# Optimization experiments

Measured on AMD Instinct MI355X. Metric: run time of the kernel, lower is better.

The kernel has to match this reference:

```python
import jax, jax.numpy as jnp
import numpy as np

N_S, N_G, D, K = 30000, 3000, 128, 16
SIGMA = 2.5
BOX = 60.0  # Angstrom box for random coordinates


def setup_inputs() -> dict:
    key = jax.random.key(0)
    ks = jax.random.split(key, 10)
    s = 1.0 / np.sqrt(D)
    return {
        'xs': jax.random.normal(ks[0], (N_S, D), jnp.float32),
        'xg': jax.random.normal(ks[1], (N_G, D), jnp.float32),
        'pos_s': jax.random.uniform(ks[2], (N_S, 3), jnp.float32) * BOX,
        'pos_g': jax.random.uniform(ks[3], (N_G, 3), jnp.float32) * BOX,
        'W_s_pre': jax.random.normal(ks[4], (D, D), jnp.float32) * s,
        'W_g_pre': jax.random.normal(ks[5], (D, D), jnp.float32) * s,
        'W_gs': jax.random.normal(ks[6], (D, D), jnp.float32) * s,
        'W_sg': jax.random.normal(ks[7], (D, D), jnp.float32) * s,
        'W_s_post': jax.random.normal(ks[8], (2 * D, D), jnp.float32) * s,
        'W_g_post': jax.random.normal(ks[9], (2 * D, D), jnp.float32) * s,
        'k': K,
    }


def reference(xs, xg, pos_s, pos_g, W_s_pre, W_g_pre, W_gs, W_sg, W_s_post, W_g_post, k):
    n_s, d = xs.shape
    # ---- compute_bipartite_graphs: knn of each graph node over surface nodes ----
    # squared pairwise distances via gemm form: (N_G, N_S)
    d2 = ((pos_g ** 2).sum(-1)[:, None] + (pos_s ** 2).sum(-1)[None, :]
          - 2.0 * pos_g @ pos_s.T)
    neg_d2, idx = jax.lax.top_k(-d2, k)          # idx: (N_G, K) surface neighbors
    w = jnp.exp(neg_d2 / (2.0 * SIGMA ** 2))     # RBF edge weight exp(-d^2/(2*sigma^2))
    # ---- pre blocks ----
    hs = xs @ W_s_pre                             # (N_S, D)
    hg = xg @ W_g_pre                             # (N_G, D)
    # ---- bp_gs block: graph -> surface weighted edge-conv (scatter-add) ----
    msg_gs = (hg @ W_gs)[:, None, :] * w[:, :, None]          # (N_G, K, D)
    xs_out = jnp.zeros((n_s, d), hs.dtype).at[idx.reshape(-1)].add(
        msg_gs.reshape(-1, d))
    # ---- bp_sg block: surface -> graph weighted edge-conv (gather-sum) ----
    xg_out = ((hs @ W_sg)[idx] * w[:, :, None]).sum(axis=1)   # (N_G, D)
    # ---- post blocks: combine pre features with message output ----
    xs_new = jax.nn.relu(jnp.concatenate([hs, xs_out], axis=-1) @ W_s_post)
    xg_new = jax.nn.relu(jnp.concatenate([hg, xg_out], axis=-1) @ W_g_post)
    return xs_new, xg_new
```

## Files before the change

kernel.cpp:

```cpp
#include <hip/hip_runtime.h>
#include <stdint.h>

#define N_S 30000
#define N_G 3000
#define DD  128
#define KK  16
#define NE  (N_G * KK)
#define NC  16
#define CELLS (NC * NC * NC)
#define CH  3.75f
#define CAP 16
#define SURV 192
#define ECAP 32
#define EOVF_CAP 8192

#define FILL_BLOCKS 118
#define PACK_BLOCKS 384
#define NBS16 1875
#define NBG16 188
#define PRE_TILES (NBS16 + NBG16)
#define GROUPS 1032
#define GRID3 (GROUPS * 5)
#define NBS 469
#define NBG 47
#define NTILE (NBS + NBG)

typedef unsigned long long ull;
#define INF_KEY 0x7F7FFFFF7FFFFFFFull

using v8s = __attribute__((ext_vector_type(8))) short;
using v4f = __attribute__((ext_vector_type(4))) float;

__device__ __forceinline__ float bf2f(unsigned short u) {
    union { unsigned int i; float f; } v; v.i = ((unsigned int)u) << 16; return v.f;
}
__device__ __forceinline__ unsigned short f2bf(float f) {
    union { float f; unsigned int i; } v; v.f = f;
    unsigned int x = v.i;
    return (unsigned short)((x + 0x7fffu + ((x >> 16) & 1u)) >> 16);
}
__device__ __forceinline__ float ldIn(const void* p, int i, int bf) {
    return bf ? bf2f(((const unsigned short*)p)[i]) : ((const float*)p)[i];
}
__device__ __forceinline__ void stOut(void* p, int i, float v, int bf) {
    if (bf) ((unsigned short*)p)[i] = f2bf(v);
    else    ((float*)p)[i] = v;
}
__device__ __forceinline__ int cellOf(float x) {
    int c = (int)(x * (1.0f / CH));
    if (c < 0) c = 0; if (c > NC - 1) c = NC - 1;
    return c;
}
__device__ __forceinline__ float dist2(float gx, float gy, float gz, float4 cd) {
    const float dx = gx - cd.x, dy = gy - cd.y, dz = gz - cd.z;
    return fmaf(dx, dx, fmaf(dy, dy, dz * dz));
}
__device__ __forceinline__ ull packKey(float d2, int sid) {
    return ((ull)__float_as_uint(d2) << 32) | (unsigned)sid;
}

__device__ __forceinline__ int detectFlag(const void* pos_g) {
    const unsigned int* w = (const unsigned int*)pos_g;
    int votes = 0;
#pragma unroll
    for (int i = 0; i < 16; ++i) {
        const unsigned int b = (w[i] >> 8) & 0xFFu;
        votes += (b >= 0x3Eu && b <= 0x42u) ? 1 : 0;
    }
    return votes >= 8;
}

__device__ __forceinline__ void emitEdge(int g, ull key, int rank,
                                         int* __restrict__ idx_out,
                                         float* __restrict__ w_out,
                                         int* __restrict__ scnt,
                                         int2* __restrict__ edge,
                                         int4* __restrict__ eovf,
                                         int* __restrict__ neovf)
{
    const int sid = (int)(unsigned)key;
    const float d2 = __uint_as_float((unsigned)(key >> 32));
    const float wv = expf(-d2 * (1.0f / 12.5f));
    idx_out[g * KK + rank] = sid;
    w_out[g * KK + rank] = wv;
    const int c = atomicAdd(&scnt[sid], 1);
    if (c < ECAP) {
        edge[(size_t)sid * ECAP + c] = make_int2(g, __float_as_int(wv));
    } else {
        const int o = atomicAdd(neovf, 1);
        if (o < EOVF_CAP) eovf[o] = make_int4(sid, g, __float_as_int(wv), 0);
    }
}

__device__ __forceinline__ void ins16(ull key, ull bk[KK]) {
    if (key >= bk[KK - 1]) return;
    ull c = key;
#pragma unroll
    for (int j = 0; j < KK; ++j) {
        const bool less = c < bk[j];
        const ull nk = less ? c : bk[j];
        const ull ok = less ? bk[j] : c;
        bk[j] = nk; c = ok;
    }
}

__device__ bool knn_fast(int g, int bf, const void* pos_g,
                         const int* __restrict__ ccnt,
                         const float4* __restrict__ scell,
                         const float4* __restrict__ ovf, int novf,
                         int* __restrict__ idx_out, float* __restrict__ w_out,
                         int* __restrict__ scnt, int2* __restrict__ edge,
                         int4* __restrict__ eovf, int* __restrict__ neovf,
                         ull* __restrict__ skey)
{
    const int t = threadIdx.x;

    const float gx = ldIn(pos_g, 3 * g + 0, bf);
    const float gy = ldIn(pos_g, 3 * g + 1, bf);
    const float gz = ldIn(pos_g, 3 * g + 2, bf);
    const int cx = cellOf(gx), cy = cellOf(gy), cz = cellOf(gz);

    float m = 1e30f;
    if (cx - 1 > 0)      m = fminf(m, gx - (float)(cx - 1) * CH);
    if (cx + 1 < NC - 1) m = fminf(m, (float)(cx + 2) * CH - gx);
    if (cy - 1 > 0)      m = fminf(m, gy - (float)(cy - 1) * CH);
    if (cy + 1 < NC - 1) m = fminf(m, (float)(cy + 2) * CH - gy);
    if (cz - 1 > 0)      m = fminf(m, gz - (float)(cz - 1) * CH);
    if (cz + 1 < NC - 1) m = fminf(m, (float)(cz + 2) * CH - gz);
    m = fmaxf(m, 0.f);
    const float m2eff = (m < 1e29f) ? m * m * (1.0f - 1e-5f) : 1e30f;

    int cnt = 0, base = 0;
    if (t < 54) {
        const int cell = t >> 1, h = t & 1;
        const int dx = cell / 9 - 1, dy = (cell / 3) % 3 - 1, dz = cell % 3 - 1;
        const int X = cx + dx, Y = cy + dy, Z = cz + dz;
        if (X >= 0 && X < NC && Y >= 0 && Y < NC && Z >= 0 && Z < NC) {
            const int cid = (X * NC + Y) * NC + Z;
            int c = ccnt[cid]; if (c > CAP) c = CAP;
            const int lo = h * 8;
            const int hi = (c < lo + 8) ? c : (lo + 8);
            cnt = (hi > lo) ? (hi - lo) : 0;
            base = cid * CAP + lo;
        }
    }

    ull kv[8]; int okm = 0;
#pragma unroll
    for (int i = 0; i < 8; ++i) {
        kv[i] = 0;
        if (i < cnt) {
            const float4 cd = scell[base + i];
            const float d2 = dist2(gx, gy, gz, cd);
            if (d2 < m2eff) { okm |= (1 << i); kv[i] = packKey(d2, __float_as_int(cd.w)); }
        }
    }
    int myc = __popc(okm);
    int incl = myc;
    for (int d = 1; d < 64; d <<= 1) {
        int v = __shfl_up(incl, d);
        if (t >= d) incl += v;
    }
    int total = __shfl(incl, 63);
    int pos = incl - myc;
#pragma unroll
    for (int i = 0; i < 8; ++i) {
        if (okm & (1 << i)) {
            if (pos < SURV) skey[pos] = kv[i];
            ++pos;
        }
    }

    for (int i0 = 0; i0 < novf; i0 += 64) {
        const int i = i0 + t;
        bool act = (i < novf);
        ull key = 0;
        if (act) {
            const float4 cd = ovf[i];
            const float d2 = dist2(gx, gy, gz, cd);
            act = (d2 < m2eff);
            if (act) key = packKey(d2, __float_as_int(cd.w));
        }
        const ull b = __ballot(act);
        const int p2 = total + (int)__popcll(b & ((1ull << t) - 1ull));
        if (act && p2 < SURV) skey[p2] = key;
        total += (int)__popcll(b);
    }

    if (total < KK || total > SURV) return false;
    __syncthreads();

    const int n = total;
    ull ki[3]; int rk[3]; int nv = 0;
    for (int i = t; i < n && nv < 3; i += 64) { ki[nv] = skey[i]; rk[nv] = 0; ++nv; }
    for (int j = 0; j < n; ++j) {
        const ull kj = skey[j];
#pragma unroll
        for (int q = 0; q < 3; ++q)
            if (q < nv) rk[q] += (kj < ki[q]) ? 1 : 0;
    }
#pragma unroll
    for (int q = 0; q < 3; ++q)
        if (q < nv && rk[q] < KK)
            emitEdge(g, ki[q], rk[q], idx_out, w_out, scnt, edge, eovf, neovf);
    return true;
}

__device__ void knn_node(int g, int bf, const void* pos_g,
                         const int* __restrict__ ccnt,
                         const float4* __restrict__ scell,
                         const float4* __restrict__ ovf, int novf,
                         int* __restrict__ idx_out, float* __restrict__ w_out,
                         int* __restrict__ scnt, int2* __restrict__ edge,
                         int4* __restrict__ eovf, int* __restrict__ neovf,
                         unsigned short* __restrict__ map16,
                         int* __restrict__ s_base, int* __restrict__ s_pref,
                         ull* __restrict__ g_key)
{
    const int t = threadIdx.x;

    const float gx = ldIn(pos_g, 3 * g + 0, bf);
    const float gy = ldIn(pos_g, 3 * g + 1, bf);
    const float gz = ldIn(pos_g, 3 * g + 2, bf);
    const int cx = cellOf(gx), cy = cellOf(gy), cz = cellOf(gz);

    ull bk[KK];
#pragma unroll
    for (int j = 0; j < KK; ++j) bk[j] = INF_KEY;

    for (int i = t; i < novf; i += 64) {
        const float4 cd = ovf[i];
        ins16(packKey(dist2(gx, gy, gz, cd), __float_as_int(cd.w)), bk);
    }

    float gk15 = 3.0e38f;
    for (int R = 1; R <= NC; ++R) {
        const int S = 2 * R + 1;
        const int Scells = S * S * S;
        for (int cb = 0; cb < Scells; cb += 64) {
            const int ci = cb + t;
            int cnt = 0, base = 0;
            if (ci < Scells) {
                const int dz = ci % S - R;
                const int dy = (ci / S) % S - R;
                const int dx = ci / (S * S) - R;
                int ax = dx < 0 ? -dx : dx, ay = dy < 0 ? -dy : dy, az = dz < 0 ? -dz : dz;
                int cheb = ax > ay ? ax : ay; if (az > cheb) cheb = az;
                const bool want = (R == 1) ? true : (cheb == R);
                const int X = cx + dx, Y = cy + dy, Z = cz + dz;
                if (want && X >= 0 && X < NC && Y >= 0 && Y < NC && Z >= 0 && Z < NC) {
                    float m2c = 0.f;
                    {
                        const float lo = (float)X * CH, hi = lo + CH;
                        const float d = (gx < lo) ? (lo - gx) : ((gx > hi) ? (gx - hi) : 0.f);
                        m2c = fmaf(d, d, m2c);
                    }
                    {
                        const float lo = (float)Y * CH, hi = lo + CH;
                        const float d = (gy < lo) ? (lo - gy) : ((gy > hi) ? (gy - hi) : 0.f);
                        m2c = fmaf(d, d, m2c);
                    }
                    {
                        const float lo = (float)Z * CH, hi = lo + CH;
                        const float d = (gz < lo) ? (lo - gz) : ((gz > hi) ? (gz - hi) : 0.f);
                        m2c = fmaf(d, d, m2c);
                    }
                    if (m2c <= gk15 * (1.0f + 1e-5f) + 1e-30f) {
                        const int cid = (X * NC + Y) * NC + Z;
                        int c = ccnt[cid]; if (c > CAP) c = CAP;
                        cnt = c; base = cid * CAP;
                    }
                }
            }
            int incl = cnt;
            for (int d = 1; d < 64; d <<= 1) {
                int v = __shfl_up(incl, d);
                if (t >= d) incl += v;
            }
            const int total = __shfl(incl, 63);
            const int pref = incl - cnt;
            s_base[t] = base; s_pref[t] = pref;
            for (int i = 0; i < cnt; ++i) map16[pref + i] = (unsigned short)t;
            __syncthreads();
            for (int pos = t; pos < total; pos += 64) {
                const int slot = map16[pos];
                const float4 cd = scell[s_base[slot] + (pos - s_pref[slot])];
                ins16(packKey(dist2(gx, gy, gz, cd), __float_as_int(cd.w)), bk);
            }
            __syncthreads();
        }
        for (int p = 0; p < KK; ++p) {
            ull key = bk[0];
            for (int d = 1; d < 64; d <<= 1) {
                const ull ok = __shfl_xor(key, d);
                if (ok < key) key = ok;
            }
            if (t == 0) g_key[p] = key;
            if (bk[0] == key) {
#pragma unroll
                for (int j = 0; j < KK - 1; ++j) bk[j] = bk[j + 1];
                bk[KK - 1] = INF_KEY;
            }
        }
        __syncthreads();
        gk15 = __uint_as_float((unsigned)(g_key[KK - 1] >> 32));
        if (t == 0) {
#pragma unroll
            for (int j = 0; j < KK; ++j) bk[j] = g_key[j];
        } else {
#pragma unroll
            for (int j = 0; j < KK; ++j) bk[j] = INF_KEY;
        }
        __syncthreads();
        float m = 1e30f;
        if (cx - R > 0)      m = fminf(m, gx - (float)(cx - R) * CH);
        if (cx + R < NC - 1) m = fminf(m, (float)(cx + R + 1) * CH - gx);
        if (cy - R > 0)      m = fminf(m, gy - (float)(cy - R) * CH);
        if (cy + R < NC - 1) m = fminf(m, (float)(cy + R + 1) * CH - gy);
        if (cz - R > 0)      m = fminf(m, gz - (float)(cz - R) * CH);
        if (cz + R < NC - 1) m = fminf(m, (float)(cz + R + 1) * CH - gz);
        m = fmaxf(m, 0.f);
        if (gk15 < m * m * (1.0f - 1e-5f)) break;
    }

    if (t == 0)
        for (int p = 0; p < KK; ++p)
            emitEdge(g, g_key[p], p, idx_out, w_out, scnt, edge, eovf, neovf);
}

__device__ __forceinline__ v8s loadA_bf16(const unsigned short* p) {
    return *(const v8s*)p;
}
__device__ __forceinline__ v8s loadA_f32v(const float* f) {
    const float4 a = *(const float4*)f;
    const float4 b = *(const float4*)(f + 4);
    v8s r;
    r[0] = (short)f2bf(a.x); r[1] = (short)f2bf(a.y);
    r[2] = (short)f2bf(a.z); r[3] = (short)f2bf(a.w);
    r[4] = (short)f2bf(b.x); r[5] = (short)f2bf(b.y);
    r[6] = (short)f2bf(b.z); r[7] = (short)f2bf(b.w);
    return r;
}
__device__ __forceinline__ v8s loadA_raw(const void* A, size_t off, int bf) {
    if (bf) return loadA_bf16((const unsigned short*)A + off);
    return loadA_f32v((const float*)A + off);
}

__device__ void pre_tile16(int task, int lane, int bf, const void* xs, const void* xg,
                           const unsigned short* __restrict__ wpk_ps,
                           const unsigned short* __restrict__ wpk_pg,
                           unsigned short* __restrict__ hsb,
                           unsigned short* __restrict__ hgb)
{
    const void* A; const unsigned short* wpk; unsigned short* outp; int M, m0;
    const bool is_s = (task < NBS16);
    if (is_s) { A = xs; wpk = wpk_ps; outp = hsb; M = N_S; m0 = task * 16; }
    else      { A = xg; wpk = wpk_pg; outp = hgb; M = N_G; m0 = (task - NBS16) * 16; }

    const int q = lane >> 4, lm = lane & 15;
    const int mrow = m0 + lm;
    const bool valid = (mrow < M);

    v4f acc[8];
#pragma unroll
    for (int t = 0; t < 8; ++t) acc[t] = {0.f, 0.f, 0.f, 0.f};
    for (int ks = 0; ks < 4; ++ks) {
        v8s a = {0,0,0,0,0,0,0,0};
        if (valid) a = loadA_raw(A, (size_t)mrow * 128 + ks * 32 + q * 8, bf);
        const unsigned short* wb = wpk + (size_t)(ks * 4 + q) * 128 * 8;
#pragma unroll
        for (int t = 0; t < 8; ++t) {
            const v8s bfr = *(const v8s*)(wb + (t * 16 + lm) * 8);
            acc[t] = __builtin_amdgcn_mfma_f32_16x16x32_bf16(a, bfr, acc[t], 0, 0, 0);
        }
    }
#pragma unroll
    for (int t = 0; t < 8; ++t)
#pragma unroll
        for (int r = 0; r < 4; ++r) {
            const int row = m0 + q * 4 + r;
            if (row < M) outp[(size_t)row * 128 + t * 16 + lm] = f2bf(acc[t][r]);
        }
}

__device__ void post_tile(int task, int bf,
                          const unsigned short* __restrict__ hsb,
                          const unsigned short* __restrict__ hgb,
                          const int* __restrict__ scnt,
                          const int2* __restrict__ edge,
                          const int4* __restrict__ eovf, int nov2,
                          const int* __restrict__ idx, const float* __restrict__ w,
                          const unsigned short* __restrict__ wpk_cs,
                          const unsigned short* __restrict__ wpk_cg,
                          void* out)
{
    const unsigned short* A1; const unsigned short* wpk;
    int M, m0, ooff;
    const bool is_s = (task < NBS);
    if (is_s) { A1 = hsb; wpk = wpk_cs; M = N_S; m0 = task * 64; ooff = 0; }
    else      { A1 = hgb; wpk = wpk_cg; M = N_G; m0 = (task - NBS) * 64; ooff = N_S * DD; }

    const int wave = threadIdx.x >> 6, lane = threadIdx.x & 63;
    const int q = lane >> 4, lm = lane & 15;
    const int mb = m0 + wave * 16;
    const int mrow = mb + lm;
    const bool valid = (mrow < M);

    v4f acc[8];
#pragma unroll
    for (int t = 0; t < 8; ++t) acc[t] = {0.f, 0.f, 0.f, 0.f};
    for (int ks = 0; ks < 8; ++ks) {
        const int kk = ks * 32 + q * 8;
        v8s a = {0,0,0,0,0,0,0,0};
        if (valid) {
            if (kk < 128) {
                a = loadA_bf16(A1 + (size_t)mrow * 128 + kk);
            } else {
                const int k2 = kk - 128;
                float f[8];
#pragma unroll
                for (int j = 0; j < 8; ++j) f[j] = 0.f;
                if (is_s) {
                    const int c = scnt[mrow];
                    const int cc = (c < ECAP) ? c : ECAP;
                    for (int e = 0; e < cc; ++e) {
                        const int2 ed = edge[(size_t)mrow * ECAP + e];
                        const float we = __int_as_float(ed.y);
                        const v8s hv = *(const v8s*)(hgb + (size_t)ed.x * 128 + k2);
#pragma unroll
                        for (int j = 0; j < 8; ++j)
                            f[j] += we * bf2f((unsigned short)hv[j]);
                    }
                    if (c > ECAP) {
                        for (int e = 0; e < nov2; ++e) {
                            const int4 ov = eovf[e];
                            if (ov.x == mrow) {
                                const float we = __int_as_float(ov.z);
                                const v8s hv = *(const v8s*)(hgb + (size_t)ov.y * 128 + k2);
#pragma unroll
                                for (int j = 0; j < 8; ++j)
                                    f[j] += we * bf2f((unsigned short)hv[j]);
                            }
                        }
                    }
                } else {
#pragma unroll 4
                    for (int e = 0; e < KK; ++e) {
                        const int gi = idx[mrow * KK + e];
                        const float we = w[mrow * KK + e];
                        const v8s hv = *(const v8s*)(hsb + (size_t)gi * 128 + k2);
#pragma unroll
                        for (int j = 0; j < 8; ++j)
                            f[j] += we * bf2f((unsigned short)hv[j]);
                    }
                }
                v8s r;
#pragma unroll
                for (int j = 0; j < 8; ++j) r[j] = (short)f2bf(f[j]);
                a = r;
            }
        }
        const unsigned short* wb = wpk + (size_t)(ks * 4 + q) * 128 * 8;
#pragma unroll
        for (int t = 0; t < 8; ++t) {
            const v8s bfr = *(const v8s*)(wb + (t * 16 + lm) * 8);
            acc[t] = __builtin_amdgcn_mfma_f32_16x16x32_bf16(a, bfr, acc[t], 0, 0, 0);
        }
    }
#pragma unroll
    for (int t = 0; t < 8; ++t)
#pragma unroll
        for (int r = 0; r < 4; ++r) {
            const int row = mb + q * 4 + r;
            if (row < M) {
                float v = acc[t][r];
                if (v < 0.f) v = 0.f;
                stOut(out, ooff + row * DD + t * 16 + lm, v, bf);
            }
        }
}

__global__ __launch_bounds__(256) void fill_pack_kernel(
    const void* pos_s, const void* pos_g,
    const void* Wsp, const void* Wgp, const void* Wgs, const void* Wsg,
    const void* Wspost, const void* Wgpost,
    int* __restrict__ ccnt, float4* __restrict__ scell,
    float4* __restrict__ ovf, int* __restrict__ novf,
    unsigned short* __restrict__ wpk_ps, unsigned short* __restrict__ wpk_pg,
    unsigned short* __restrict__ wpk_cs, unsigned short* __restrict__ wpk_cg)
{
    const int bf = detectFlag(pos_g);
    const int bid = blockIdx.x, tid = threadIdx.x;
    if (bid < FILL_BLOCKS) {
        const int p = bid * 256 + tid;
        if (p < N_S) {
            const float x = ldIn(pos_s, 3 * p + 0, bf);
            const float y = ldIn(pos_s, 3 * p + 1, bf);
            const float z = ldIn(pos_s, 3 * p + 2, bf);
            const int cid = (cellOf(x) * NC + cellOf(y)) * NC + cellOf(z);
            const int slot = atomicAdd(&ccnt[cid], 1);
            const float4 pt = make_float4(x, y, z, __int_as_float(p));
            if (slot < CAP) scell[cid * CAP + slot] = pt;
            else            ovf[atomicAdd(novf, 1)] = pt;
        }
        return;
    }
    __shared__ float rows[256];
    const int rt = bid - FILL_BLOCKS;
    const int half = tid >> 7, j = tid & 127;
    const int task = rt * 2 + half;
    float v; unsigned short* dst; int k;
    if (task < 128) { k = task; v = ldIn(Wsp, k * DD + j, bf); dst = wpk_ps; }
    else if (task < 256) { k = task - 128; v = ldIn(Wgp, k * DD + j, bf); dst = wpk_pg; }
    else {
        const int which_g = (task >= 512);
        const int r = which_g ? (task - 512) : (task - 256);
        const void* W1 = which_g ? Wsg : Wgs;
        const void* Wp = which_g ? Wgpost : Wspost;
        dst = which_g ? wpk_cg : wpk_cs;
        k = r;
        if (r < 128) v = ldIn(Wp, r * DD + j, bf);
        else {
            rows[half * 128 + j] = ldIn(W1, (r - 128) * DD + j, bf);
            __syncthreads();
            float acc = 0.f;
            for (int m = 0; m < DD; ++m)
                acc += rows[half * 128 + m] * ldIn(Wp, (DD + m) * DD + j, bf);
            v = acc;
        }
    }
    const int ks = k >> 5, q = (k >> 3) & 3, i = k & 7;
    dst[((ks * 4 + q) * 128 + j) * 8 + i] = f2bf(v);
}

__global__ __launch_bounds__(64) void knn_pre_kernel(
    const void* xs, const void* xg, const void* pos_g,
    const int* __restrict__ ccnt, const float4* __restrict__ scell,
    const float4* __restrict__ ovf, const int* __restrict__ novf,
    int* __restrict__ idx, float* __restrict__ w,
    int* __restrict__ scnt, int2* __restrict__ edge,
    int4* __restrict__ eovf, int* __restrict__ neovf,
    const unsigned short* __restrict__ wpk_ps,
    const unsigned short* __restrict__ wpk_pg,
    unsigned short* __restrict__ hsb, unsigned short* __restrict__ hgb)
{
    const int bf = detectFlag(pos_g);
    const int bid = blockIdx.x;
    const int group = bid / 5, off = bid - group * 5;
    if (off < 3) {
        const int g = group * 3 + off;
        if (g >= N_G) return;
        __shared__ ull skey[SURV];
        const int nov = *novf;
        if (!knn_fast(g, bf, pos_g, ccnt, scell, ovf, nov, idx, w,
                      scnt, edge, eovf, neovf, skey)) {
            __shared__ unsigned short map16[64 * CAP];
            __shared__ int s_base[64];
            __shared__ int s_pref[64];
            __shared__ ull g_key[KK];
            __syncthreads();
            knn_node(g, bf, pos_g, ccnt, scell, ovf, nov, idx, w,
                     scnt, edge, eovf, neovf, map16, s_base, s_pref, g_key);
        }
    } else {
        const int task = group * 2 + (off - 3);
        if (task >= PRE_TILES) return;
        pre_tile16(task, threadIdx.x, bf, xs, xg, wpk_ps, wpk_pg, hsb, hgb);
    }
}

__global__ __launch_bounds__(256) void mfma_post_kernel(
    const void* pos_g,
    const unsigned short* __restrict__ hsb, const unsigned short* __restrict__ hgb,
    const int* __restrict__ scnt, const int2* __restrict__ edge,
    const int4* __restrict__ eovf, const int* __restrict__ neovf,
    const int* __restrict__ idx, const float* __restrict__ w,
    const unsigned short* __restrict__ wpk_cs, const unsigned short* __restrict__ wpk_cg,
    void* out)
{
    const int bf = detectFlag(pos_g);
    int nov2 = *neovf; if (nov2 > EOVF_CAP) nov2 = EOVF_CAP;
    post_tile(blockIdx.x, bf, hsb, hgb, scnt, edge, eovf, nov2,
              idx, w, wpk_cs, wpk_cg, out);
}

extern "C" void kernel_launch(void* const* d_in, const int* in_sizes, int n_in,
                              void* d_out, int out_size, void* d_ws, size_t ws_size,
                              hipStream_t stream)
{
    const void* xs       = d_in[0];
    const void* xg       = d_in[1];
    const void* pos_s    = d_in[2];
    const void* pos_g    = d_in[3];
    const void* W_s_pre  = d_in[4];
    const void* W_g_pre  = d_in[5];
    const void* W_gs     = d_in[6];
    const void* W_sg     = d_in[7];
    const void* W_s_post = d_in[8];
    const void* W_g_post = d_in[9];
    (void)in_sizes; (void)n_in; (void)out_size; (void)ws_size;

    char* ws = (char*)d_ws;
    size_t off_b = 0;
    auto alloc = [&](size_t bytes) -> void* {
        void* p = ws + off_b;
        off_b = (off_b + bytes + 255) & ~((size_t)255);
        return p;
    };
    unsigned short* hsb    = (unsigned short*)alloc((size_t)N_S * DD * 2);
    unsigned short* hgb    = (unsigned short*)alloc((size_t)N_G * DD * 2);
    unsigned short* wpk_ps = (unsigned short*)alloc((size_t)DD * DD * 2);
    unsigned short* wpk_pg = (unsigned short*)alloc((size_t)DD * DD * 2);
    unsigned short* wpk_cs = (unsigned short*)alloc((size_t)2 * DD * DD * 2);
    unsigned short* wpk_cg = (unsigned short*)alloc((size_t)2 * DD * DD * 2);
    int*            idx    = (int*)   alloc((size_t)NE * 4);
    float*          w      = (float*) alloc((size_t)NE * 4);
    int*            ibase  = (int*)   alloc((size_t)(CELLS + 1 + N_S + 1) * 4);
    int*            ccnt   = ibase;
    int*            novf   = ibase + CELLS;
    int*            scnt   = ibase + CELLS + 1;
    int*            neovf  = ibase + CELLS + 1 + N_S;
    float4*         scell  = (float4*)alloc((size_t)CELLS * CAP * 16);
    float4*         ovf    = (float4*)alloc((size_t)N_S * 16);
    int2*           edge   = (int2*)  alloc((size_t)N_S * ECAP * 8);
    int4*           eovf   = (int4*)  alloc((size_t)EOVF_CAP * 16);

    hipMemsetAsync(ibase, 0, (size_t)(CELLS + 1 + N_S + 1) * 4, stream);

    fill_pack_kernel<<<FILL_BLOCKS + PACK_BLOCKS, 256, 0, stream>>>(
        pos_s, pos_g, W_s_pre, W_g_pre, W_gs, W_sg, W_s_post, W_g_post,
        ccnt, scell, ovf, novf, wpk_ps, wpk_pg, wpk_cs, wpk_cg);

    knn_pre_kernel<<<GRID3, 64, 0, stream>>>(
        xs, xg, pos_g, ccnt, scell, ovf, novf, idx, w,
        scnt, edge, eovf, neovf, wpk_ps, wpk_pg, hsb, hgb);

    mfma_post_kernel<<<NTILE, 256, 0, stream>>>(
        pos_g, hsb, hgb, scnt, edge, eovf, neovf, idx, w,
        wpk_cs, wpk_cg, d_out);
}
```

Measured before the change: 169.7 us.

## Replace two-path kNN with single wave-level register top-k and hoist edge gather

Drops the shared-memory fast path (survivor list plus rank counting) and the LDS-based fallback, and replaces both with one wave-only kNN. Each lane keeps its own sorted top-16 in registers, candidates are reduced with shuffles, and there is no shared memory and no __syncthreads. This also drops the per-cell pruning against the current 16th distance. In the post GEMM, the weighted neighbour gather for the message half is done once per row up front instead of inside the k-slice loop, and the launch bounds now ask for 4 waves per SIMD. In exchange, every lane always runs the 16-deep insertion sort on up to 8 points per shell, which can cost more than the old rank counting for the common case. The larger register arrays may also spill under the occupancy hint.

Result: slower. 181.2 us (+6.8%).

```diff
diff --git a/kernel.cpp b/kernel.cpp
--- a/kernel.cpp
+++ b/kernel.cpp
@@ -10,7 +10,6 @@
 #define CELLS (NC * NC * NC)
 #define CH  3.75f
 #define CAP 16
-#define SURV 192
 #define ECAP 32
 #define EOVF_CAP 8192
 
@@ -104,14 +103,13 @@
     }
 }
 
-__device__ bool knn_fast(int g, int bf, const void* pos_g,
+__device__ void knn_wave(int g, int bf, const void* pos_g,
                          const int* __restrict__ ccnt,
                          const float4* __restrict__ scell,
                          const float4* __restrict__ ovf, int novf,
                          int* __restrict__ idx_out, float* __restrict__ w_out,
                          int* __restrict__ scnt, int2* __restrict__ edge,
-                         int4* __restrict__ eovf, int* __restrict__ neovf,
-                         ull* __restrict__ skey)
+                         int4* __restrict__ eovf, int* __restrict__ neovf)
 {
     const int t = threadIdx.x;
 
@@ -120,198 +118,75 @@
     const float gz = ldIn(pos_g, 3 * g + 2, bf);
     const int cx = cellOf(gx), cy = cellOf(gy), cz = cellOf(gz);
 
-    float m = 1e30f;
-    if (cx - 1 > 0)      m = fminf(m, gx - (float)(cx - 1) * CH);
-    if (cx + 1 < NC - 1) m = fminf(m, (float)(cx + 2) * CH - gx);
-    if (cy - 1 > 0)      m = fminf(m, gy - (float)(cy - 1) * CH);
-    if (cy + 1 < NC - 1) m = fminf(m, (float)(cy + 2) * CH - gy);
-    if (cz - 1 > 0)      m = fminf(m, gz - (float)(cz - 1) * CH);
-    if (cz + 1 < NC - 1) m = fminf(m, (float)(cz + 2) * CH - gz);
-    m = fmaxf(m, 0.f);
-    const float m2eff = (m < 1e29f) ? m * m * (1.0f - 1e-5f) : 1e30f;
-
-    int cnt = 0, base = 0;
-    if (t < 54) {
-        const int cell = t >> 1, h = t & 1;
-        const int dx = cell / 9 - 1, dy = (cell / 3) % 3 - 1, dz = cell % 3 - 1;
-        const int X = cx + dx, Y = cy + dy, Z = cz + dz;
-        if (X >= 0 && X < NC && Y >= 0 && Y < NC && Z >= 0 && Z < NC) {
-            const int cid = (X * NC + Y) * NC + Z;
-            int c = ccnt[cid]; if (c > CAP) c = CAP;
-            const int lo = h * 8;
-            const int hi = (c < lo + 8) ? c : (lo + 8);
-            cnt = (hi > lo) ? (hi - lo) : 0;
-            base = cid * CAP + lo;
-        }
-    }
-
-    ull kv[8]; int okm = 0;
-#pragma unroll
-    for (int i = 0; i < 8; ++i) {
-        kv[i] = 0;
-        if (i < cnt) {
-            const float4 cd = scell[base + i];
-            const float d2 = dist2(gx, gy, gz, cd);
-            if (d2 < m2eff) { okm |= (1 << i); kv[i] = packKey(d2, __float_as_int(cd.w)); }
-        }
-    }
-    int myc = __popc(okm);
-    int incl = myc;
-    for (int d = 1; d < 64; d <<= 1) {
-        int v = __shfl_up(incl, d);
-        if (t >= d) incl += v;
-    }
-    int total = __shfl(incl, 63);
-    int pos = incl - myc;
-#pragma unroll
-    for (int i = 0; i < 8; ++i) {
-        if (okm & (1 << i)) {
-            if (pos < SURV) skey[pos] = kv[i];
-            ++pos;
-        }
-    }
+    ull bk[KK];
+#pragma unroll
+    for (int j = 0; j < KK; ++j) bk[j] = INF_KEY;
 
     for (int i0 = 0; i0 < novf; i0 += 64) {
         const int i = i0 + t;
-        bool act = (i < novf);
-        ull key = 0;
-        if (act) {
+        if (i < novf) {
             const float4 cd = ovf[i];
-            const float d2 = dist2(gx, gy, gz, cd);
-            act = (d2 < m2eff);
-            if (act) key = packKey(d2, __float_as_int(cd.w));
-        }
-        const ull b = __ballot(act);
-        const int p2 = total + (int)__popcll(b & ((1ull << t) - 1ull));
-        if (act && p2 < SURV) skey[p2] = key;
-        total += (int)__popcll(b);
-    }
-
-    if (total < KK || total > SURV) return false;
-    __syncthreads();
-
-    const int n = total;
-    ull ki[3]; int rk[3]; int nv = 0;
-    for (int i = t; i < n && nv < 3; i += 64) { ki[nv] = skey[i]; rk[nv] = 0; ++nv; }
-    for (int j = 0; j < n; ++j) {
-        const ull kj = skey[j];
-#pragma unroll
-        for (int q = 0; q < 3; ++q)
-            if (q < nv) rk[q] += (kj < ki[q]) ? 1 : 0;
-    }
-#pragma unroll
-    for (int q = 0; q < 3; ++q)
-        if (q < nv && rk[q] < KK)
-            emitEdge(g, ki[q], rk[q], idx_out, w_out, scnt, edge, eovf, neovf);
-    return true;
-}
-
-__device__ void knn_node(int g, int bf, const void* pos_g,
-                         const int* __restrict__ ccnt,
-                         const float4* __restrict__ scell,
-                         const float4* __restrict__ ovf, int novf,
-                         int* __restrict__ idx_out, float* __restrict__ w_out,
-                         int* __restrict__ scnt, int2* __restrict__ edge,
-                         int4* __restrict__ eovf, int* __restrict__ neovf,
-                         unsigned short* __restrict__ map16,
-                         int* __restrict__ s_base, int* __restrict__ s_pref,
-                         ull* __restrict__ g_key)
-{
-    const int t = threadIdx.x;
-
-    const float gx = ldIn(pos_g, 3 * g + 0, bf);
-    const float gy = ldIn(pos_g, 3 * g + 1, bf);
-    const float gz = ldIn(pos_g, 3 * g + 2, bf);
-    const int cx = cellOf(gx), cy = cellOf(gy), cz = cellOf(gz);
-
-    ull bk[KK];
-#pragma unroll
-    for (int j = 0; j < KK; ++j) bk[j] = INF_KEY;
-
-    for (int i = t; i < novf; i += 64) {
-        const float4 cd = ovf[i];
-        ins16(packKey(dist2(gx, gy, gz, cd), __float_as_int(cd.w)), bk);
-    }
-
-    float gk15 = 3.0e38f;
+            ins16(packKey(dist2(gx, gy, gz, cd), __float_as_int(cd.w)), bk);
+        }
+    }
+
+    ull myKey = INF_KEY;
     for (int R = 1; R <= NC; ++R) {
         const int S = 2 * R + 1;
-        const int Scells = S * S * S;
-        for (int cb = 0; cb < Scells; cb += 64) {
-            const int ci = cb + t;
+        const int S3 = S * S * S;
+        for (int b0 = 0; b0 < 2 * S3; b0 += 64) {
+            const int pt = b0 + t;
             int cnt = 0, base = 0;
-            if (ci < Scells) {
-                const int dz = ci % S - R;
-                const int dy = (ci / S) % S - R;
-                const int dx = ci / (S * S) - R;
-                int ax = dx < 0 ? -dx : dx, ay = dy < 0 ? -dy : dy, az = dz < 0 ? -dz : dz;
+            if (pt < 2 * S3) {
+                const int cell = pt >> 1, h = pt & 1;
+                int dx, dy, dz;
+                if (R == 1) {
+                    dx = cell / 9 - 1; dy = (cell / 3) % 3 - 1; dz = cell % 3 - 1;
+                } else {
+                    dx = cell / (S * S) - R; dy = (cell / S) % S - R; dz = cell % S - R;
+                }
+                const int ax = dx < 0 ? -dx : dx, ay = dy < 0 ? -dy : dy,
+                          az = dz < 0 ? -dz : dz;
                 int cheb = ax > ay ? ax : ay; if (az > cheb) cheb = az;
-                const bool want = (R == 1) ? true : (cheb == R);
+                const bool want = (R == 1) || (cheb == R);
                 const int X = cx + dx, Y = cy + dy, Z = cz + dz;
                 if (want && X >= 0 && X < NC && Y >= 0 && Y < NC && Z >= 0 && Z < NC) {
-                    float m2c = 0.f;
-                    {
-                        const float lo = (float)X * CH, hi = lo + CH;
-                        const float d = (gx < lo) ? (lo - gx) : ((gx > hi) ? (gx - hi) : 0.f);
-                        m2c = fmaf(d, d, m2c);
-                    }
-                    {
-                        const float lo = (float)Y * CH, hi = lo + CH;
-                        const float d = (gy < lo) ? (lo - gy) : ((gy > hi) ? (gy - hi) : 0.f);
-                        m2c = fmaf(d, d, m2c);
-                    }
-                    {
-                        const float lo = (float)Z * CH, hi = lo + CH;
-                        const float d = (gz < lo) ? (lo - gz) : ((gz > hi) ? (gz - hi) : 0.f);
-                        m2c = fmaf(d, d, m2c);
-                    }
-                    if (m2c <= gk15 * (1.0f + 1e-5f) + 1e-30f) {
-                        const int cid = (X * NC + Y) * NC + Z;
-                        int c = ccnt[cid]; if (c > CAP) c = CAP;
-                        cnt = c; base = cid * CAP;
-                    }
+                    const int cid = (X * NC + Y) * NC + Z;
+                    int c = ccnt[cid]; if (c > CAP) c = CAP;
+                    const int lo = h * 8;
+                    const int hi = (c < lo + 8) ? c : (lo + 8);
+                    cnt = (hi > lo) ? (hi - lo) : 0;
+                    base = cid * CAP + lo;
                 }
             }
-            int incl = cnt;
-            for (int d = 1; d < 64; d <<= 1) {
-                int v = __shfl_up(incl, d);
-                if (t >= d) incl += v;
-            }
-            const int total = __shfl(incl, 63);
-            const int pref = incl - cnt;
-            s_base[t] = base; s_pref[t] = pref;
-            for (int i = 0; i < cnt; ++i) map16[pref + i] = (unsigned short)t;
-            __syncthreads();
-            for (int pos = t; pos < total; pos += 64) {
-                const int slot = map16[pos];
-                const float4 cd = scell[s_base[slot] + (pos - s_pref[slot])];
-                ins16(packKey(dist2(gx, gy, gz, cd), __float_as_int(cd.w)), bk);
-            }
-            __syncthreads();
-        }
+            float4 cds[8];
+#pragma unroll
+            for (int i = 0; i < 8; ++i)
+                if (i < cnt) cds[i] = scell[base + i];
+#pragma unroll
+            for (int i = 0; i < 8; ++i)
+                if (i < cnt)
+                    ins16(packKey(dist2(gx, gy, gz, cds[i]),
+                                  __float_as_int(cds[i].w)), bk);
+        }
+
+        myKey = INF_KEY;
         for (int p = 0; p < KK; ++p) {
             ull key = bk[0];
             for (int d = 1; d < 64; d <<= 1) {
                 const ull ok = __shfl_xor(key, d);
                 if (ok < key) key = ok;
             }
-            if (t == 0) g_key[p] = key;
+            if (t == p) myKey = key;
             if (bk[0] == key) {
 #pragma unroll
                 for (int j = 0; j < KK - 1; ++j) bk[j] = bk[j + 1];
                 bk[KK - 1] = INF_KEY;
             }
         }
-        __syncthreads();
-        gk15 = __uint_as_float((unsigned)(g_key[KK - 1] >> 32));
-        if (t == 0) {
-#pragma unroll
-            for (int j = 0; j < KK; ++j) bk[j] = g_key[j];
-        } else {
-#pragma unroll
-            for (int j = 0; j < KK; ++j) bk[j] = INF_KEY;
-        }
-        __syncthreads();
+
+        const ull k15 = __shfl(myKey, KK - 1);
+        const float d15 = __uint_as_float((unsigned)(k15 >> 32));
         float m = 1e30f;
         if (cx - R > 0)      m = fminf(m, gx - (float)(cx - R) * CH);
         if (cx + R < NC - 1) m = fminf(m, (float)(cx + R + 1) * CH - gx);
@@ -320,12 +195,14 @@
         if (cz - R > 0)      m = fminf(m, gz - (float)(cz - R) * CH);
         if (cz + R < NC - 1) m = fminf(m, (float)(cz + R + 1) * CH - gz);
         m = fmaxf(m, 0.f);
-        if (gk15 < m * m * (1.0f - 1e-5f)) break;
-    }
-
-    if (t == 0)
-        for (int p = 0; p < KK; ++p)
-            emitEdge(g, g_key[p], p, idx_out, w_out, scnt, edge, eovf, neovf);
+        const float m2eff = (m < 1e29f) ? m * m * (1.0f - 1e-5f) : 1e30f;
+        if (d15 < m2eff || R == NC) break;
+
+        if (t < KK && myKey != INF_KEY) ins16(myKey, bk);
+    }
+
+    if (t < KK)
+        emitEdge(g, myKey, t, idx_out, w_out, scnt, edge, eovf, neovf);
 }
 
 __device__ __forceinline__ v8s loadA_bf16(const unsigned short* p) {
@@ -406,59 +283,82 @@
     const int mrow = mb + lm;
     const bool valid = (mrow < M);
 
+    v8s a2[4];
+    if (valid) {
+        float f[4][8];
+#pragma unroll
+        for (int si = 0; si < 4; ++si)
+#pragma unroll
+            for (int j = 0; j < 8; ++j) f[si][j] = 0.f;
+        if (is_s) {
+            const int c = scnt[mrow];
+            const int cc = (c < ECAP) ? c : ECAP;
+            for (int e = 0; e < cc; ++e) {
+                const int2 ed = edge[(size_t)mrow * ECAP + e];
+                const float we = __int_as_float(ed.y);
+                const unsigned short* hrow = hgb + (size_t)ed.x * 128 + q * 8;
+#pragma unroll
+                for (int si = 0; si < 4; ++si) {
+                    const v8s hv = *(const v8s*)(hrow + si * 32);
+#pragma unroll
+                    for (int j = 0; j < 8; ++j)
+                        f[si][j] += we * bf2f((unsigned short)hv[j]);
+                }
+            }
+            if (c > ECAP) {
+                for (int e = 0; e < nov2; ++e) {
+                    const int4 ov = eovf[e];
+                    if (ov.x == mrow) {
+                        const float we = __int_as_float(ov.z);
+                        const unsigned short* hrow = hgb + (size_t)ov.y * 128 + q * 8;
+#pragma unroll
+                        for (int si = 0; si < 4; ++si) {
+                            const v8s hv = *(const v8s*)(hrow + si * 32);
+#pragma unroll
+                            for (int j = 0; j < 8; ++j)
+                                f[si][j] += we * bf2f((unsigned short)hv[j]);
+                        }
+                    }
+                }
+            }
+        } else {
+            for (int e = 0; e < KK; ++e) {
+                const int gi = idx[mrow * KK + e];
+                const float we = w[mrow * KK + e];
+                const unsigned short* hrow = hsb + (size_t)gi * 128 + q * 8;
+#pragma unroll
+                for (int si = 0; si < 4; ++si) {
+                    const v8s hv = *(const v8s*)(hrow + si * 32);
+#pragma unroll
+                    for (int j = 0; j < 8; ++j)
+                        f[si][j] += we * bf2f((unsigned short)hv[j]);
+                }
+            }
+        }
+#pragma unroll
+        for (int si = 0; si < 4; ++si) {
+            v8s r;
+#pragma unroll
+            for (int j = 0; j < 8; ++j) r[j] = (short)f2bf(f[si][j]);
+            a2[si] = r;
+        }
+    } else {
+#pragma unroll
+        for (int si = 0; si < 4; ++si) a2[si] = (v8s){0,0,0,0,0,0,0,0};
+    }
+
     v4f acc[8];
 #pragma unroll
     for (int t = 0; t < 8; ++t) acc[t] = {0.f, 0.f, 0.f, 0.f};
+#pragma unroll
     for (int ks = 0; ks < 8; ++ks) {
         const int kk = ks * 32 + q * 8;
-        v8s a = {0,0,0,0,0,0,0,0};
-        if (valid) {
-            if (kk < 128) {
-                a = loadA_bf16(A1 + (size_t)mrow * 128 + kk);
-            } else {
-                const int k2 = kk - 128;
-                float f[8];
-#pragma unroll
-                for (int j = 0; j < 8; ++j) f[j] = 0.f;
-                if (is_s) {
-                    const int c = scnt[mrow];
-                    const int cc = (c < ECAP) ? c : ECAP;
-                    for (int e = 0; e < cc; ++e) {
-                        const int2 ed = edge[(size_t)mrow * ECAP + e];
-                        const float we = __int_as_float(ed.y);
-                        const v8s hv = *(const v8s*)(hgb + (size_t)ed.x * 128 + k2);
-#pragma unroll
-                        for (int j = 0; j < 8; ++j)
-                            f[j] += we * bf2f((unsigned short)hv[j]);
-                    }
-                    if (c > ECAP) {
-                        for (int e = 0; e < nov2; ++e) {
-                            const int4 ov = eovf[e];
-                            if (ov.x == mrow) {
-                                const float we = __int_as_float(ov.z);
-                                const v8s hv = *(const v8s*)(hgb + (size_t)ov.y * 128 + k2);
-#pragma unroll
-                                for (int j = 0; j < 8; ++j)
-                                    f[j] += we * bf2f((unsigned short)hv[j]);
-                            }
-                        }
-                    }
-                } else {
-#pragma unroll 4
-                    for (int e = 0; e < KK; ++e) {
-                        const int gi = idx[mrow * KK + e];
-                        const float we = w[mrow * KK + e];
-                        const v8s hv = *(const v8s*)(hsb + (size_t)gi * 128 + k2);
-#pragma unroll
-                        for (int j = 0; j < 8; ++j)
-                            f[j] += we * bf2f((unsigned short)hv[j]);
-                    }
-                }
-                v8s r;
-#pragma unroll
-                for (int j = 0; j < 8; ++j) r[j] = (short)f2bf(f[j]);
-                a = r;
-            }
+        v8s a;
+        if (ks < 4) {
+            a = (v8s){0,0,0,0,0,0,0,0};
+            if (valid) a = loadA_bf16(A1 + (size_t)mrow * 128 + kk);
+        } else {
+            a = a2[ks - 4];
         }
         const unsigned short* wb = wpk + (size_t)(ks * 4 + q) * 128 * 8;
 #pragma unroll
@@ -533,7 +433,7 @@
     dst[((ks * 4 + q) * 128 + j) * 8 + i] = f2bf(v);
 }
 
-__global__ __launch_bounds__(64) void knn_pre_kernel(
+__global__ __launch_bounds__(64, 4) void knn_pre_kernel(
     const void* xs, const void* xg, const void* pos_g,
     const int* __restrict__ ccnt, const float4* __restrict__ scell,
     const float4* __restrict__ ovf, const int* __restrict__ novf,
@@ -550,18 +450,9 @@
     if (off < 3) {
         const int g = group * 3 + off;
         if (g >= N_G) return;
-        __shared__ ull skey[SURV];
         const int nov = *novf;
-        if (!knn_fast(g, bf, pos_g, ccnt, scell, ovf, nov, idx, w,
-                      scnt, edge, eovf, neovf, skey)) {
-            __shared__ unsigned short map16[64 * CAP];
-            __shared__ int s_base[64];
-            __shared__ int s_pref[64];
-            __shared__ ull g_key[KK];
-            __syncthreads();
-            knn_node(g, bf, pos_g, ccnt, scell, ovf, nov, idx, w,
-                     scnt, edge, eovf, neovf, map16, s_base, s_pref, g_key);
-        }
+        knn_wave(g, bf, pos_g, ccnt, scell, ovf, nov, idx, w,
+                 scnt, edge, eovf, neovf);
     } else {
         const int task = group * 2 + (off - 3);
         if (task >= PRE_TILES) return;
```

## Hoist edge gather out of K loop and replace barrier with lgkmcnt wait

Applied to the files above, without the earlier changes.

The post-block GEMM used to walk each row's edge list four separate times, once per upper K-slice, with the index and weight loads repeated every time. It now walks the edge list once and accumulates all four 32-column slices into a register array before the MFMA loop, which is now fully unrolled. Separately, the __syncthreads in the kNN candidate ranking becomes a plain s_waitcnt lgkmcnt(0). That is only safe if the ranking block is a single wavefront, and it relies on LDS ordering within that wave. The gather hoist raises register pressure (32 float accumulators plus four held fragments), which may reduce occupancy.

New measurement: 173.0 us. Within noise of the previous version (+1.9%).

```diff
diff --git a/kernel.cpp b/kernel.cpp
--- a/kernel.cpp
+++ b/kernel.cpp
@@ -188,7 +188,8 @@
     }
 
     if (total < KK || total > SURV) return false;
-    __syncthreads();
+
+    asm volatile("s_waitcnt lgkmcnt(0)" ::: "memory");
 
     const int n = total;
     ull ki[3]; int rk[3]; int nv = 0;
@@ -406,59 +407,82 @@
     const int mrow = mb + lm;
     const bool valid = (mrow < M);
 
+    v8s a2[4];
+    if (valid) {
+        float f[4][8];
+#pragma unroll
+        for (int si = 0; si < 4; ++si)
+#pragma unroll
+            for (int j = 0; j < 8; ++j) f[si][j] = 0.f;
+        if (is_s) {
+            const int c = scnt[mrow];
+            const int cc = (c < ECAP) ? c : ECAP;
+            for (int e = 0; e < cc; ++e) {
+                const int2 ed = edge[(size_t)mrow * ECAP + e];
+                const float we = __int_as_float(ed.y);
+                const unsigned short* hrow = hgb + (size_t)ed.x * 128 + q * 8;
+#pragma unroll
+                for (int si = 0; si < 4; ++si) {
+                    const v8s hv = *(const v8s*)(hrow + si * 32);
+#pragma unroll
+                    for (int j = 0; j < 8; ++j)
+                        f[si][j] += we * bf2f((unsigned short)hv[j]);
+                }
+            }
+            if (c > ECAP) {
+                for (int e = 0; e < nov2; ++e) {
+                    const int4 ov = eovf[e];
+                    if (ov.x == mrow) {
+                        const float we = __int_as_float(ov.z);
+                        const unsigned short* hrow = hgb + (size_t)ov.y * 128 + q * 8;
+#pragma unroll
+                        for (int si = 0; si < 4; ++si) {
+                            const v8s hv = *(const v8s*)(hrow + si * 32);
+#pragma unroll
+                            for (int j = 0; j < 8; ++j)
+                                f[si][j] += we * bf2f((unsigned short)hv[j]);
+                        }
+                    }
+                }
+            }
+        } else {
+            for (int e = 0; e < KK; ++e) {
+                const int gi = idx[mrow * KK + e];
+                const float we = w[mrow * KK + e];
+                const unsigned short* hrow = hsb + (size_t)gi * 128 + q * 8;
+#pragma unroll
+                for (int si = 0; si < 4; ++si) {
+                    const v8s hv = *(const v8s*)(hrow + si * 32);
+#pragma unroll
+                    for (int j = 0; j < 8; ++j)
+                        f[si][j] += we * bf2f((unsigned short)hv[j]);
+                }
+            }
+        }
+#pragma unroll
+        for (int si = 0; si < 4; ++si) {
+            v8s r;
+#pragma unroll
+            for (int j = 0; j < 8; ++j) r[j] = (short)f2bf(f[si][j]);
+            a2[si] = r;
+        }
+    } else {
+#pragma unroll
+        for (int si = 0; si < 4; ++si) a2[si] = (v8s){0,0,0,0,0,0,0,0};
+    }
+
     v4f acc[8];
 #pragma unroll
     for (int t = 0; t < 8; ++t) acc[t] = {0.f, 0.f, 0.f, 0.f};
+#pragma unroll
     for (int ks = 0; ks < 8; ++ks) {
         const int kk = ks * 32 + q * 8;
-        v8s a = {0,0,0,0,0,0,0,0};
-        if (valid) {
-            if (kk < 128) {
-                a = loadA_bf16(A1 + (size_t)mrow * 128 + kk);
-            } else {
-                const int k2 = kk - 128;
-                float f[8];
-#pragma unroll
-                for (int j = 0; j < 8; ++j) f[j] = 0.f;
-                if (is_s) {
-                    const int c = scnt[mrow];
-                    const int cc = (c < ECAP) ? c : ECAP;
-                    for (int e = 0; e < cc; ++e) {
-                        const int2 ed = edge[(size_t)mrow * ECAP + e];
-                        const float we = __int_as_float(ed.y);
-                        const v8s hv = *(const v8s*)(hgb + (size_t)ed.x * 128 + k2);
-#pragma unroll
-                        for (int j = 0; j < 8; ++j)
-                            f[j] += we * bf2f((unsigned short)hv[j]);
-                    }
-                    if (c > ECAP) {
-                        for (int e = 0; e < nov2; ++e) {
-                            const int4 ov = eovf[e];
-                            if (ov.x == mrow) {
-                                const float we = __int_as_float(ov.z);
-                                const v8s hv = *(const v8s*)(hgb + (size_t)ov.y * 128 + k2);
-#pragma unroll
-                                for (int j = 0; j < 8; ++j)
-                                    f[j] += we * bf2f((unsigned short)hv[j]);
-                            }
-                        }
-                    }
-                } else {
-#pragma unroll 4
-                    for (int e = 0; e < KK; ++e) {
-                        const int gi = idx[mrow * KK + e];
-                        const float we = w[mrow * KK + e];
-                        const v8s hv = *(const v8s*)(hsb + (size_t)gi * 128 + k2);
-#pragma unroll
-                        for (int j = 0; j < 8; ++j)
-                            f[j] += we * bf2f((unsigned short)hv[j]);
-                    }
-                }
-                v8s r;
-#pragma unroll
-                for (int j = 0; j < 8; ++j) r[j] = (short)f2bf(f[j]);
-                a = r;
-            }
+        v8s a;
+        if (ks < 4) {
+            a = (v8s){0,0,0,0,0,0,0,0};
+            if (valid) a = loadA_bf16(A1 + (size_t)mrow * 128 + kk);
+        } else {
+            a = a2[ks - 4];
         }
         const unsigned short* wb = wpk + (size_t)(ks * 4 + q) * 128 * 8;
 #pragma unroll
```
